# Kernel optimization log

Measured on AMD Instinct MI355X. Metric: run time of the kernel, lower is better.

## Reference

```python
import jax, jax.numpy as jnp
import numpy as np

# SMPL kinematic tree: parent index of each of the 24 joints (root's parent unused)
PARENTS = (0, 0, 0, 0, 1, 2, 3, 4, 5, 6, 7, 8, 9, 9, 9, 12, 13, 14, 16, 17, 18, 19, 20, 21)
NUM_JOINTS = 24
BATCH = 131072


def setup_inputs() -> dict:
    key = jax.random.key(0)
    k1, k2 = jax.random.split(key)
    joint_rotations = jax.random.normal(k1, (BATCH, NUM_JOINTS, 3, 3), dtype=jnp.float32)
    joint_positions = jax.random.normal(k2, (BATCH, NUM_JOINTS, 3), dtype=jnp.float32)
    return {"joint_rotations": joint_rotations, "joint_positions": joint_positions}


def reference(joint_rotations, joint_positions):
    B = joint_rotations.shape[0]
    J = NUM_JOINTS
    pos = joint_positions[..., None]  # [B, J, 3, 1]

    # Relative (bone-local) translations: root keeps absolute position.
    parents_arr = jnp.asarray(PARENTS, dtype=jnp.int32)
    rel = pos - pos[:, parents_arr]            # [B, J, 3, 1]; rel[:,0] == 0
    rel = rel.at[:, 0].set(pos[:, 0])          # root uses absolute position

    # Build all local affine transforms at once: [B, J, 4, 4]
    rot_homo = jnp.pad(joint_rotations, ((0, 0), (0, 0), (0, 1), (0, 0)))  # [B,J,4,3]
    trans_homo = jnp.concatenate([rel, jnp.ones((B, J, 1, 1), rel.dtype)], axis=2)  # [B,J,4,1]
    local = jnp.concatenate([rot_homo, trans_homo], axis=3)  # [B,J,4,4]

    # Sequential parent-to-child chain over the static tree (23 tiny batched matmuls).
    transforms = [local[:, 0]]
    for j in range(1, J):
        transforms.append(jnp.matmul(transforms[PARENTS[j]], local[:, j]))
    transforms = jnp.stack(transforms, axis=1)  # [B, J, 4, 4]

    joint_positions_posed = transforms[:, :, :3, 3]  # [B, J, 3]

    # Subtract the transform applied to the rest pose (standard SMPL trick).
    zeros = jnp.zeros((B, J, 1, 1), pos.dtype)
    joint_rest = jnp.concatenate([pos, zeros], axis=2)   # [B, J, 4, 1]
    init_bone = jnp.matmul(transforms, joint_rest)       # [B, J, 4, 1]
    init_bone = jnp.pad(init_bone, ((0, 0), (0, 0), (0, 0), (3, 0)))  # [B, J, 4, 4]
    joint_transforms = transforms - init_bone
    return (joint_transforms, joint_positions_posed)
```

## Files before the change

kernel.cpp:

```cpp
#include <hip/hip_runtime.h>

namespace {
constexpr int NB  = 131072;
constexpr int NJ  = 24;
constexpr int PAR[NJ] = {0,0,0,0,1,2,3,4,5,6,7,8,9,9,9,12,13,14,16,17,18,19,20,21};
constexpr int BLK = 64;
constexpr int SOT = 68;
constexpr int SPO = 76;
constexpr int LDSF = BLK * SPO;
}

typedef float f32x4 __attribute__((ext_vector_type(4)));

__global__ __launch_bounds__(BLK) void pose_kernel(
    const float* __restrict__ rot,
    const float* __restrict__ pos,
    float* __restrict__ outT,
    float* __restrict__ outP)
{
    __shared__ __align__(16) float lds[LDSF];
    const int t  = threadIdx.x;
    const int b0 = blockIdx.x * BLK;

    const float* prow = pos + (size_t)(b0 + t) * 72;
    const float* rrow = rot + (size_t)(b0 + t) * 216;

    float Rg[NJ][9];
    float tg[NJ][3];
    float carry1[9];
    float carry2[6];

    #pragma unroll
    for (int g = 0; g < 3; ++g) {
        float Pg[24];
        #pragma unroll
        for (int i = 0; i < 6; ++i) {
            f32x4 v = *reinterpret_cast<const f32x4*>(prow + 24 * g + 4 * i);
            Pg[4*i+0] = v.x; Pg[4*i+1] = v.y; Pg[4*i+2] = v.z; Pg[4*i+3] = v.w;
        }

        #pragma unroll
        for (int q = 0; q < 2; ++q) {
            float buf[36];
            #pragma unroll
            for (int i = 0; i < 9; ++i) {
                f32x4 v = *reinterpret_cast<const f32x4*>(rrow + 72 * g + 36 * q + 4 * i);
                buf[4*i+0] = v.x; buf[4*i+1] = v.y; buf[4*i+2] = v.z; buf[4*i+3] = v.w;
            }

            #pragma unroll
            for (int l = 0; l < 4; ++l) {
                const int j  = 8 * g + 4 * q + l;
                const int pj = PAR[j];
                float L[9];
                #pragma unroll
                for (int k = 0; k < 9; ++k) L[k] = buf[9 * (4 * q + l) - 36 * q + k];

                if (j == 0) {
                    #pragma unroll
                    for (int k = 0; k < 9; ++k) Rg[0][k] = L[k];
                    tg[0][0] = Pg[0]; tg[0][1] = Pg[1]; tg[0][2] = Pg[2];
                } else {
                    float pxp, pyp, pzp;
                    if (pj >= 8 * g) {
                        const int lp = 3 * pj - 24 * g;
                        pxp = Pg[lp]; pyp = Pg[lp+1]; pzp = Pg[lp+2];
                    } else if (g == 1) {
                        const int ci = 3 * (pj - 5);
                        pxp = carry1[ci]; pyp = carry1[ci+1]; pzp = carry1[ci+2];
                    } else {
                        const int ci = 3 * (pj - 13);
                        pxp = carry2[ci]; pyp = carry2[ci+1]; pzp = carry2[ci+2];
                    }
                    const int lj = 3 * j - 24 * g;
                    float rel[3] = { Pg[lj] - pxp, Pg[lj+1] - pyp, Pg[lj+2] - pzp };
                    #pragma unroll
                    for (int r = 0; r < 3; ++r) {
                        #pragma unroll
                        for (int c = 0; c < 3; ++c) {
                            Rg[j][3*r+c] = Rg[pj][3*r+0] * L[0+c]
                                         + Rg[pj][3*r+1] * L[3+c]
                                         + Rg[pj][3*r+2] * L[6+c];
                        }
                        tg[j][r] = Rg[pj][3*r+0] * rel[0]
                                 + Rg[pj][3*r+1] * rel[1]
                                 + Rg[pj][3*r+2] * rel[2]
                                 + tg[pj][r];
                    }
                }
            }

            #pragma unroll
            for (int l = 0; l < 4; ++l) {
                const int j  = 8 * g + 4 * q + l;
                const int lj = 3 * j - 24 * g;
                float px = Pg[lj], py = Pg[lj+1], pz = Pg[lj+2];
                #pragma unroll
                for (int r = 0; r < 3; ++r) {
                    float ib = Rg[j][3*r]*px + Rg[j][3*r+1]*py + Rg[j][3*r+2]*pz;
                    *reinterpret_cast<f32x4*>(&lds[t * SOT + (l*4 + r) * 4]) =
                        f32x4{Rg[j][3*r], Rg[j][3*r+1], Rg[j][3*r+2], tg[j][r] - ib};
                }
                *reinterpret_cast<f32x4*>(&lds[t * SOT + (l*4 + 3) * 4]) =
                    f32x4{0.f, 0.f, 0.f, 1.f};
            }
            {
                float* gp = outT + (size_t)b0 * 384 + (8 * g + 4 * q) * 16;
                #pragma unroll
                for (int i = 0; i < 16; ++i) {
                    int f = t + BLK * i;
                    int row = f >> 4, col = f & 15;
                    f32x4 v = *reinterpret_cast<const f32x4*>(&lds[row * SOT + col * 4]);
                    __builtin_nontemporal_store(
                        v, reinterpret_cast<f32x4*>(gp + (size_t)row * 384 + col * 4));
                }
            }
        }

        if (g == 0) {
            #pragma unroll
            for (int k = 0; k < 9; ++k) carry1[k] = Pg[15 + k];
        } else if (g == 1) {
            #pragma unroll
            for (int k = 0; k < 6; ++k) carry2[k] = Pg[15 + k];
        }
    }

    #pragma unroll
    for (int i = 0; i < 18; ++i) {
        float vals[4];
        #pragma unroll
        for (int k = 0; k < 4; ++k) {
            int e = 4*i + k;
            vals[k] = tg[e / 3][e % 3];
        }
        *reinterpret_cast<f32x4*>(&lds[t * SPO + i * 4]) =
            f32x4{vals[0], vals[1], vals[2], vals[3]};
    }
    {
        float* gp = outP + (size_t)b0 * 72;
        #pragma unroll
        for (int i = 0; i < 18; ++i) {
            int f = t + BLK * i;
            int row = f / 18, col = f % 18;
            f32x4 v = *reinterpret_cast<const f32x4*>(&lds[row * SPO + col * 4]);
            __builtin_nontemporal_store(
                v, reinterpret_cast<f32x4*>(gp + (size_t)row * 72 + col * 4));
        }
    }
}

extern "C" void kernel_launch(void* const* d_in, const int* in_sizes, int n_in,
                              void* d_out, int out_size, void* d_ws, size_t ws_size,
                              hipStream_t stream) {
    const float* rot = (const float*)d_in[0];
    const float* pos = (const float*)d_in[1];
    float* outT = (float*)d_out;
    float* outP = outT + (size_t)NB * NJ * 16;
    dim3 grid(NB / BLK), block(BLK);
    hipLaunchKernelGGL(pose_kernel, grid, block, 0, stream, rot, pos, outT, outP);
}
```

Measured before the change: 66.61 us.

## Split compute and store into producer/consumer waves with double-buffered LDS

Each block now has two waves. One wave computes the transform chain and writes results for two joints at a time into a double-buffered LDS area. The other wave waits on barriers and streams each staged chunk to global memory with nontemporal stores. The goal is to overlap the serial compute with the output writes, at the cost of a barrier per chunk and an idle wave that occupies a slot. The barrier schedule has to line up exactly: 12 transform phases plus 2 position phases on both sides.

Result: slower. 104.4 us (+56.7%).

```diff
diff --git a/kernel.cpp b/kernel.cpp
--- a/kernel.cpp
+++ b/kernel.cpp
@@ -4,148 +4,176 @@
 constexpr int NB  = 131072;
 constexpr int NJ  = 24;
 constexpr int PAR[NJ] = {0,0,0,0,1,2,3,4,5,6,7,8,9,9,9,12,13,14,16,17,18,19,20,21};
-constexpr int BLK = 64;
-constexpr int SOT = 68;
-constexpr int SPO = 76;
-constexpr int LDSF = BLK * SPO;
+constexpr int BLK = 128;
+constexpr int BPB = 64;
+constexpr int STR = 9;
+constexpr int NF4 = BPB * STR;
 }
 
 typedef float f32x4 __attribute__((ext_vector_type(4)));
 
-__global__ __launch_bounds__(BLK) void pose_kernel(
+__device__ __forceinline__ void sync_lds() {
+    __builtin_amdgcn_sched_barrier(0);
+    asm volatile("s_waitcnt lgkmcnt(0)" ::: "memory");
+    __builtin_amdgcn_s_barrier();
+    __builtin_amdgcn_sched_barrier(0);
+}
+
+__global__ __launch_bounds__(BLK, 4) void pose_kernel(
     const float* __restrict__ rot,
     const float* __restrict__ pos,
     float* __restrict__ outT,
     float* __restrict__ outP)
 {
-    __shared__ __align__(16) float lds[LDSF];
-    const int t  = threadIdx.x;
-    const int b0 = blockIdx.x * BLK;
+    __shared__ __align__(16) f32x4 lds[2 * NF4];
+    const int t    = threadIdx.x;
+    const int lane = t & 63;
+    const int wv   = t >> 6;
+    const int b0   = blockIdx.x * BPB;
 
-    const float* prow = pos + (size_t)(b0 + t) * 72;
-    const float* rrow = rot + (size_t)(b0 + t) * 216;
+    if (wv == 0) {
+        const float* prow = pos + (size_t)(b0 + lane) * 72;
+        const float* rrow = rot + (size_t)(b0 + lane) * 216;
 
-    float Rg[NJ][9];
-    float tg[NJ][3];
-    float carry1[9];
-    float carry2[6];
+        float Rg[NJ][9];
+        float tg[NJ][3];
+        float carry1[9];
+        float carry2[6];
 
-    #pragma unroll
-    for (int g = 0; g < 3; ++g) {
-        float Pg[24];
         #pragma unroll
-        for (int i = 0; i < 6; ++i) {
-            f32x4 v = *reinterpret_cast<const f32x4*>(prow + 24 * g + 4 * i);
-            Pg[4*i+0] = v.x; Pg[4*i+1] = v.y; Pg[4*i+2] = v.z; Pg[4*i+3] = v.w;
+        for (int g = 0; g < 3; ++g) {
+            float Pg[24];
+            #pragma unroll
+            for (int i = 0; i < 6; ++i) {
+                f32x4 v = *reinterpret_cast<const f32x4*>(prow + 24 * g + 4 * i);
+                Pg[4*i+0] = v.x; Pg[4*i+1] = v.y; Pg[4*i+2] = v.z; Pg[4*i+3] = v.w;
+            }
+
+            #pragma unroll
+            for (int q = 0; q < 2; ++q) {
+                float buf[36];
+                #pragma unroll
+                for (int i = 0; i < 9; ++i) {
+                    f32x4 v = *reinterpret_cast<const f32x4*>(rrow + 72*g + 36*q + 4*i);
+                    buf[4*i+0] = v.x; buf[4*i+1] = v.y; buf[4*i+2] = v.z; buf[4*i+3] = v.w;
+                }
+
+                #pragma unroll
+                for (int l = 0; l < 4; ++l) {
+                    const int j  = 8 * g + 4 * q + l;
+                    const int pj = PAR[j];
+                    const float* L = buf + 9 * l;
+
+                    if (j == 0) {
+                        #pragma unroll
+                        for (int k = 0; k < 9; ++k) Rg[0][k] = L[k];
+                        tg[0][0] = Pg[0]; tg[0][1] = Pg[1]; tg[0][2] = Pg[2];
+                    } else {
+                        float pxp, pyp, pzp;
+                        if (pj >= 8 * g) {
+                            const int lp = 3 * pj - 24 * g;
+                            pxp = Pg[lp]; pyp = Pg[lp+1]; pzp = Pg[lp+2];
+                        } else if (g == 1) {
+                            const int ci = 3 * (pj - 5);
+                            pxp = carry1[ci]; pyp = carry1[ci+1]; pzp = carry1[ci+2];
+                        } else {
+                            const int ci = 3 * (pj - 13);
+                            pxp = carry2[ci]; pyp = carry2[ci+1]; pzp = carry2[ci+2];
+                        }
+                        const int lj = 3 * j - 24 * g;
+                        float rel[3] = { Pg[lj] - pxp, Pg[lj+1] - pyp, Pg[lj+2] - pzp };
+                        #pragma unroll
+                        for (int r = 0; r < 3; ++r) {
+                            #pragma unroll
+                            for (int c = 0; c < 3; ++c) {
+                                Rg[j][3*r+c] = Rg[pj][3*r+0] * L[0+c]
+                                             + Rg[pj][3*r+1] * L[3+c]
+                                             + Rg[pj][3*r+2] * L[6+c];
+                            }
+                            tg[j][r] = Rg[pj][3*r+0] * rel[0]
+                                     + Rg[pj][3*r+1] * rel[1]
+                                     + Rg[pj][3*r+2] * rel[2]
+                                     + tg[pj][r];
+                        }
+                    }
+                }
+
+                #pragma unroll
+                for (int hp = 0; hp < 2; ++hp) {
+                    const int p = 4 * g + 2 * q + hp;
+                    f32x4* B = &lds[(p & 1) * NF4 + lane * STR];
+                    #pragma unroll
+                    for (int jj = 0; jj < 2; ++jj) {
+                        const int j  = 8 * g + 4 * q + 2 * hp + jj;
+                        const int lj = 3 * j - 24 * g;
+                        const float px = Pg[lj], py = Pg[lj+1], pz = Pg[lj+2];
+                        #pragma unroll
+                        for (int r = 0; r < 3; ++r) {
+                            const float ib = Rg[j][3*r]*px + Rg[j][3*r+1]*py
+                                           + Rg[j][3*r+2]*pz;
+                            B[jj*4 + r] = f32x4{Rg[j][3*r], Rg[j][3*r+1],
+                                                Rg[j][3*r+2], tg[j][r] - ib};
+                        }
+                        B[jj*4 + 3] = f32x4{0.f, 0.f, 0.f, 1.f};
+                    }
+                    sync_lds();
+                }
+            }
+
+            if (g == 0) {
+                #pragma unroll
+                for (int k = 0; k < 9; ++k) carry1[k] = Pg[15 + k];
+            } else if (g == 1) {
+                #pragma unroll
+                for (int k = 0; k < 6; ++k) carry2[k] = Pg[15 + k];
+            }
         }
 
         #pragma unroll
-        for (int q = 0; q < 2; ++q) {
-            float buf[36];
+        for (int ph = 0; ph < 2; ++ph) {
+            const int p = 12 + ph;
+            f32x4* B = &lds[(p & 1) * NF4 + lane * STR];
             #pragma unroll
             for (int i = 0; i < 9; ++i) {
-                f32x4 v = *reinterpret_cast<const f32x4*>(rrow + 72 * g + 36 * q + 4 * i);
-                buf[4*i+0] = v.x; buf[4*i+1] = v.y; buf[4*i+2] = v.z; buf[4*i+3] = v.w;
+                float vals[4];
+                #pragma unroll
+                for (int k = 0; k < 4; ++k) {
+                    int e = 36 * ph + 4 * i + k;
+                    vals[k] = tg[e / 3][e % 3];
+                }
+                B[i] = f32x4{vals[0], vals[1], vals[2], vals[3]};
             }
-
+            sync_lds();
+        }
+    } else {
+        #pragma unroll
+        for (int p = 0; p < 12; ++p) {
+            sync_lds();
+            const f32x4* B = &lds[(p & 1) * NF4];
+            float* gp = outT + (size_t)b0 * 384 + p * 32;
             #pragma unroll
-            for (int l = 0; l < 4; ++l) {
-                const int j  = 8 * g + 4 * q + l;
-                const int pj = PAR[j];
-                float L[9];
-                #pragma unroll
-                for (int k = 0; k < 9; ++k) L[k] = buf[9 * (4 * q + l) - 36 * q + k];
-
-                if (j == 0) {
-                    #pragma unroll
-                    for (int k = 0; k < 9; ++k) Rg[0][k] = L[k];
-                    tg[0][0] = Pg[0]; tg[0][1] = Pg[1]; tg[0][2] = Pg[2];
-                } else {
-                    float pxp, pyp, pzp;
-                    if (pj >= 8 * g) {
-                        const int lp = 3 * pj - 24 * g;
-                        pxp = Pg[lp]; pyp = Pg[lp+1]; pzp = Pg[lp+2];
-                    } else if (g == 1) {
-                        const int ci = 3 * (pj - 5);
-                        pxp = carry1[ci]; pyp = carry1[ci+1]; pzp = carry1[ci+2];
-                    } else {
-                        const int ci = 3 * (pj - 13);
-                        pxp = carry2[ci]; pyp = carry2[ci+1]; pzp = carry2[ci+2];
-                    }
-                    const int lj = 3 * j - 24 * g;
-                    float rel[3] = { Pg[lj] - pxp, Pg[lj+1] - pyp, Pg[lj+2] - pzp };
-                    #pragma unroll
-                    for (int r = 0; r < 3; ++r) {
-                        #pragma unroll
-                        for (int c = 0; c < 3; ++c) {
-                            Rg[j][3*r+c] = Rg[pj][3*r+0] * L[0+c]
-                                         + Rg[pj][3*r+1] * L[3+c]
-                                         + Rg[pj][3*r+2] * L[6+c];
-                        }
-                        tg[j][r] = Rg[pj][3*r+0] * rel[0]
-                                 + Rg[pj][3*r+1] * rel[1]
-                                 + Rg[pj][3*r+2] * rel[2]
-                                 + tg[pj][r];
-                    }
-                }
-            }
-
-            #pragma unroll
-            for (int l = 0; l < 4; ++l) {
-                const int j  = 8 * g + 4 * q + l;
-                const int lj = 3 * j - 24 * g;
-                float px = Pg[lj], py = Pg[lj+1], pz = Pg[lj+2];
-                #pragma unroll
-                for (int r = 0; r < 3; ++r) {
-                    float ib = Rg[j][3*r]*px + Rg[j][3*r+1]*py + Rg[j][3*r+2]*pz;
-                    *reinterpret_cast<f32x4*>(&lds[t * SOT + (l*4 + r) * 4]) =
-                        f32x4{Rg[j][3*r], Rg[j][3*r+1], Rg[j][3*r+2], tg[j][r] - ib};
-                }
-                *reinterpret_cast<f32x4*>(&lds[t * SOT + (l*4 + 3) * 4]) =
-                    f32x4{0.f, 0.f, 0.f, 1.f};
-            }
-            {
-                float* gp = outT + (size_t)b0 * 384 + (8 * g + 4 * q) * 16;
-                #pragma unroll
-                for (int i = 0; i < 16; ++i) {
-                    int f = t + BLK * i;
-                    int row = f >> 4, col = f & 15;
-                    f32x4 v = *reinterpret_cast<const f32x4*>(&lds[row * SOT + col * 4]);
-                    __builtin_nontemporal_store(
-                        v, reinterpret_cast<f32x4*>(gp + (size_t)row * 384 + col * 4));
-                }
+            for (int i = 0; i < 8; ++i) {
+                int f = lane + 64 * i;
+                int row = f >> 3, col = f & 7;
+                f32x4 v = B[row * STR + col];
+                __builtin_nontemporal_store(
+                    v, reinterpret_cast<f32x4*>(gp + (size_t)row * 384 + col * 4));
             }
         }
-
-        if (g == 0) {
+        #pragma unroll
+        for (int ph = 0; ph < 2; ++ph) {
+            const int p = 12 + ph;
+            sync_lds();
+            const f32x4* B = &lds[(p & 1) * NF4];
+            float* gp = outP + (size_t)b0 * 72 + ph * 36;
             #pragma unroll
-            for (int k = 0; k < 9; ++k) carry1[k] = Pg[15 + k];
-        } else if (g == 1) {
-            #pragma unroll
-            for (int k = 0; k < 6; ++k) carry2[k] = Pg[15 + k];
-        }
-    }
-
-    #pragma unroll
-    for (int i = 0; i < 18; ++i) {
-        float vals[4];
-        #pragma unroll
-        for (int k = 0; k < 4; ++k) {
-            int e = 4*i + k;
-            vals[k] = tg[e / 3][e % 3];
-        }
-        *reinterpret_cast<f32x4*>(&lds[t * SPO + i * 4]) =
-            f32x4{vals[0], vals[1], vals[2], vals[3]};
-    }
-    {
-        float* gp = outP + (size_t)b0 * 72;
-        #pragma unroll
-        for (int i = 0; i < 18; ++i) {
-            int f = t + BLK * i;
-            int row = f / 18, col = f % 18;
-            f32x4 v = *reinterpret_cast<const f32x4*>(&lds[row * SPO + col * 4]);
-            __builtin_nontemporal_store(
-                v, reinterpret_cast<f32x4*>(gp + (size_t)row * 72 + col * 4));
+            for (int i = 0; i < 9; ++i) {
+                int f = lane + 64 * i;
+                int row = f / 9, col = f % 9;
+                f32x4 v = B[row * STR + col];
+                __builtin_nontemporal_store(
+                    v, reinterpret_cast<f32x4*>(gp + (size_t)row * 72 + col * 4));
+            }
         }
     }
 }
@@ -157,6 +185,6 @@
     const float* pos = (const float*)d_in[1];
     float* outT = (float*)d_out;
     float* outP = outT + (size_t)NB * NJ * 16;
-    dim3 grid(NB / BLK), block(BLK);
+    dim3 grid(NB / BPB), block(BLK);
     hipLaunchKernelGGL(pose_kernel, grid, block, 0, stream, rot, pos, outT, outP);
 }
```
